# Kernel tuning notes

Measured on AMD Instinct MI355X. Metric: run time of the kernel, lower is better.

The kernel has to match this reference:

```python
import jax, jax.numpy as jnp
import numpy as np
from jax import lax

B, IMG, P, D, DEPTH = 32, 512, 16, 256, 8
G = IMG // P            # 32 grid side
N = G * G               # 1024 tokens
DQ = D // 8             # 32 (CCNet-style reduced q/k dim)
DF = 4 * D

# fixed Laplacian kernel for EdgeTokenExtractor (depthwise, HWIO with I=1)
_LAP = np.array([[0., -1., 0.], [-1., 4., -1.], [0., -1., 0.]], np.float32)


def setup_inputs() -> dict:
    key = jax.random.key(0)
    ks = jax.random.split(key, 16)
    s = 0.02
    return {
        'x': jax.random.normal(ks[0], (B, 1, IMG, IMG), jnp.float32),
        'w_patch': jax.random.normal(ks[1], (D, 1, P, P), jnp.float32) * s,
        'b_patch': jnp.zeros((D,), jnp.float32),
        'pos': jax.random.normal(ks[2], (1, N, D), jnp.float32) * s,
        'w_edge': jax.random.normal(ks[3], (D, D), jnp.float32) * s,
        'b_edge': jnp.zeros((D,), jnp.float32),
        'ln_g': jnp.ones((DEPTH, D), jnp.float32),
        'ln_b': jnp.zeros((DEPTH, D), jnp.float32),
        'wq': jax.random.normal(ks[4], (DEPTH, D, DQ), jnp.float32) * s,
        'bq': jnp.zeros((DEPTH, DQ), jnp.float32),
        'wk': jax.random.normal(ks[5], (DEPTH, D, DQ), jnp.float32) * s,
        'bk': jnp.zeros((DEPTH, DQ), jnp.float32),
        'wv': jax.random.normal(ks[6], (DEPTH, D, D), jnp.float32) * s,
        'bv': jnp.zeros((DEPTH, D), jnp.float32),
        'gamma': jnp.full((DEPTH,), 0.1, jnp.float32),
        'w1': jax.random.normal(ks[7], (DEPTH, D, DF), jnp.float32) * s,
        'b1': jnp.zeros((DEPTH, DF), jnp.float32),
        'w2': jax.random.normal(ks[8], (DEPTH, DF, D), jnp.float32) * s,
        'b2': jnp.zeros((DEPTH, D), jnp.float32),
        'w_head': jax.random.normal(ks[9], (D, 1), jnp.float32) * s,
        'b_head': jnp.zeros((1,), jnp.float32),
    }


def _ln(x, g, b):
    m = x.mean(-1, keepdims=True)
    v = ((x - m) ** 2).mean(-1, keepdims=True)
    return (x - m) * lax.rsqrt(v + 1e-5) * g + b


def _criss_cross(xn, wq, bq, wk, bk, wv, bv, gamma):
    # xn: [B,N,D] -> grid [B,G,G,D]; each token attends to its row + column.
    b_ = xn.shape[0]
    grid = xn.reshape(b_, G, G, D)
    q = grid @ wq + bq            # [B,G,G,DQ]
    k = grid @ wk + bk
    v = grid @ wv + bv            # [B,G,G,D]
    scale = 1.0 / np.sqrt(DQ).astype(np.float32)
    row = jnp.einsum('bhwc,bhvc->bhwv', q, k) * scale   # attend along width
    col = jnp.einsum('bhwc,buwc->bhwu', q, k) * scale   # attend along height
    # mask the duplicated self position in the column branch (CCNet trick)
    col = col - 1e9 * jnp.eye(G, dtype=col.dtype)[:, None, :]
    a = jax.nn.softmax(jnp.concatenate([row, col], axis=-1), axis=-1)  # [B,G,G,2G]
    out = (jnp.einsum('bhwv,bhvc->bhwc', a[..., :G], v)
           + jnp.einsum('bhwu,buwc->bhwc', a[..., G:], v))
    return (gamma * out + grid).reshape(b_, N, D)


def _edge_tokens(t, w_edge, b_edge):
    # depthwise Laplacian over the token grid, then linear + tanh
    b_ = t.shape[0]
    grid = t.reshape(b_, G, G, D)
    kern = jnp.tile(jnp.asarray(_LAP).reshape(3, 3, 1, 1), (1, 1, 1, D))  # [3,3,1,D]
    e = lax.conv_general_dilated(grid, kern, (1, 1), 'SAME',
                                 dimension_numbers=('NHWC', 'HWIO', 'NHWC'),
                                 feature_group_count=D)
    return jnp.tanh(e.reshape(b_, N, D) @ w_edge + b_edge)


def reference(x, w_patch, b_patch, pos, w_edge, b_edge, ln_g, ln_b,
              wq, bq, wk, bk, wv, bv, gamma, w1, b1, w2, b2, w_head, b_head):
    b_ = x.shape[0]
    # patch embed: conv stride=patch -> [B,D,G,G] -> [B,N,D]
    t = lax.conv_general_dilated(x, w_patch, (P, P), 'VALID',
                                 dimension_numbers=('NCHW', 'OIHW', 'NCHW'))
    t = t + b_patch[None, :, None, None]
    t = t.reshape(b_, D, N).transpose(0, 2, 1)
    t = t + pos
    t = t + _edge_tokens(t, w_edge, b_edge)

    def block(h, p):
        lg, lb, wq_, bq_, wk_, bk_, wv_, bv_, gm, w1_, b1_, w2_, b2_ = p
        # NOTE: original block reuses the SAME LayerNorm params for both sublayers
        h = h + _criss_cross(_ln(h, lg, lb), wq_, bq_, wk_, bk_, wv_, bv_, gm)
        hn = _ln(h, lg, lb)
        h = h + jax.nn.gelu(hn @ w1_ + b1_, approximate=False) @ w2_ + b2_
        return h, None

    t, _ = lax.scan(block, t, (ln_g, ln_b, wq, bq, wk, bk, wv, bv, gamma, w1, b1, w2, b2))
    out = t @ w_head + b_head                      # [B,N,1]
    return out.transpose(0, 2, 1).reshape(b_, 1, G, G)
```

## Files before the change

### kernel.cpp

```cpp
#include <hip/hip_runtime.h>
#include <hip/hip_bf16.h>

#define BB   32
#define IMG  512
#define PP   16
#define DD   256
#define GG   32
#define NN   1024
#define DQ_  32
#define DF_  1024
#define DEPTH_ 8

using short8  = __attribute__((ext_vector_type(8))) short;
using floatx4 = __attribute__((ext_vector_type(4))) float;

__device__ __forceinline__ float bu2f(unsigned short u) {
    return __uint_as_float(((unsigned int)u) << 16);
}
__device__ __forceinline__ unsigned short f2b(float f) {
    unsigned int u = __float_as_uint(f);
    u += 0x7fffu + ((u >> 16) & 1u);
    return (unsigned short)(u >> 16);
}
__device__ __forceinline__ float gelu_exact(float x) {
    return 0.5f * x * (1.0f + erff(x * 0.70710678118654752440f));
}
__device__ __forceinline__ float lo16(unsigned int u) {
    return __uint_as_float(u << 16);
}
__device__ __forceinline__ float hi16(unsigned int u) {
    return __uint_as_float(u & 0xffff0000u);
}
__device__ __forceinline__ float dot8(uint4 a, uint4 b) {
    const unsigned int* pa = (const unsigned int*)&a;
    const unsigned int* pb = (const unsigned int*)&b;
    float s = 0.f;
    #pragma unroll
    for (int i = 0; i < 4; ++i)
        s += lo16(pa[i]) * lo16(pb[i]) + hi16(pa[i]) * hi16(pb[i]);
    return s;
}

__global__ __launch_bounds__(256) void k_wtrans(const float* __restrict__ in,
                                                unsigned short* __restrict__ out,
                                                int R, int C) {
    __shared__ float tile[32][33];
    const int l = blockIdx.z;
    const int r0 = blockIdx.x * 32, c0 = blockIdx.y * 32;
    const int tx = threadIdx.x & 31, ty = threadIdx.x >> 5;
    const float* src = in + (size_t)l * R * C;
    unsigned short* dst = out + (size_t)l * R * C;
    #pragma unroll
    for (int i = 0; i < 4; ++i)
        tile[ty + i * 8][tx] = src[(size_t)(r0 + ty + i * 8) * C + c0 + tx];
    __syncthreads();
    #pragma unroll
    for (int i = 0; i < 4; ++i)
        dst[(size_t)(c0 + ty + i * 8) * R + r0 + tx] = f2b(tile[tx][ty + i * 8]);
}

__global__ __launch_bounds__(256) void k_qktrans(const float* __restrict__ wq,
                                                 const float* __restrict__ wk,
                                                 unsigned short* __restrict__ o) {
    const int l = blockIdx.z, j = blockIdx.x, k = threadIdx.x;
    float v = (j < 32) ? wq[(size_t)l * 8192 + k * 32 + j]
                       : wk[(size_t)l * 8192 + k * 32 + (j - 32)];
    o[((size_t)l * 64 + j) * 256 + k] = f2b(v);
}

__global__ void k_bqk(const float* __restrict__ bq, const float* __restrict__ bk,
                      float* __restrict__ o) {
    const int l = blockIdx.x, j = threadIdx.x;
    o[l * 64 + j] = (j < 32) ? bq[l * 32 + j] : bk[l * 32 + (j - 32)];
}

__global__ __launch_bounds__(256) void k_cvt(const float* __restrict__ in,
                                             unsigned short* __restrict__ out) {
    int i = blockIdx.x * 256 + threadIdx.x;
    out[i] = f2b(in[i]);
}

__global__ __launch_bounds__(256) void k_im2col(const float* __restrict__ x,
                                                unsigned short* __restrict__ xp) {
    const int tok = blockIdx.x;
    const int b  = tok >> 10;
    const int n  = tok & (NN - 1);
    const int gi = n >> 5, gj = n & 31;
    const int pi = threadIdx.x >> 4, pj = threadIdx.x & 15;
    xp[(size_t)tok * 256 + threadIdx.x] =
        f2b(x[(size_t)(b * IMG + gi * PP + pi) * IMG + gj * PP + pj]);
}

template <int K, int N, int MODE>
__global__ __launch_bounds__(256) void k_gemm(
    const unsigned short* __restrict__ A, const unsigned short* __restrict__ Bt,
    const float* __restrict__ bias, unsigned short* __restrict__ Cb,
    float* __restrict__ Cf, const float* __restrict__ pos) {
    __shared__ alignas(16) unsigned short As[64 * 32];
    __shared__ alignas(16) unsigned short Bs[64 * 32];
    const int t  = threadIdx.x;
    const int m0 = blockIdx.x * 64, n0 = blockIdx.y * 64;
    const int row = t >> 2, ch = t & 3;
    const unsigned short* ga = A  + (size_t)(m0 + row) * K + ch * 8;
    const unsigned short* gb = Bt + (size_t)(n0 + row) * K + ch * 8;

    const int lane = t & 63, wid = t >> 6;
    const int quad = lane >> 4, r = lane & 15;
    const int wm = (wid >> 1) * 32, wn = (wid & 1) * 32;

    floatx4 acc00 = {0.f, 0.f, 0.f, 0.f}, acc01 = {0.f, 0.f, 0.f, 0.f};
    floatx4 acc10 = {0.f, 0.f, 0.f, 0.f}, acc11 = {0.f, 0.f, 0.f, 0.f};

    uint4 ra = *(const uint4*)ga;
    uint4 rb = *(const uint4*)gb;
    const int KS = K / 32;
    for (int ks = 0; ks < KS; ++ks) {
        __syncthreads();
        *(uint4*)&As[t * 8] = ra;
        *(uint4*)&Bs[t * 8] = rb;
        __syncthreads();
        if (ks + 1 < KS) {
            ra = *(const uint4*)(ga + (ks + 1) * 32);
            rb = *(const uint4*)(gb + (ks + 1) * 32);
        }
        short8 a0 = *(const short8*)&As[(wm + r) * 32 + quad * 8];
        short8 a1 = *(const short8*)&As[(wm + 16 + r) * 32 + quad * 8];
        short8 b0 = *(const short8*)&Bs[(wn + r) * 32 + quad * 8];
        short8 b1 = *(const short8*)&Bs[(wn + 16 + r) * 32 + quad * 8];
        acc00 = __builtin_amdgcn_mfma_f32_16x16x32_bf16(a0, b0, acc00, 0, 0, 0);
        acc01 = __builtin_amdgcn_mfma_f32_16x16x32_bf16(a0, b1, acc01, 0, 0, 0);
        acc10 = __builtin_amdgcn_mfma_f32_16x16x32_bf16(a1, b0, acc10, 0, 0, 0);
        acc11 = __builtin_amdgcn_mfma_f32_16x16x32_bf16(a1, b1, acc11, 0, 0, 0);
    }
    const int nA = n0 + wn + r;
    const int nB = nA + 16;
    const float bias0 = bias[nA], bias1 = bias[nB];
    #pragma unroll
    for (int i = 0; i < 2; ++i) {
        floatx4 aj0 = i ? acc10 : acc00;
        floatx4 aj1 = i ? acc11 : acc01;
        const int mb = m0 + wm + i * 16 + quad * 4;
        #pragma unroll
        for (int g = 0; g < 4; ++g) {
            const int m = mb + g;
            float v0 = aj0[g] + bias0, v1 = aj1[g] + bias1;
            if (MODE == 0) {
                Cb[(size_t)m * N + nA] = f2b(gelu_exact(v0));
                Cb[(size_t)m * N + nB] = f2b(gelu_exact(v1));
            } else if (MODE == 1) {
                Cf[(size_t)m * N + nA] += v0;
                Cf[(size_t)m * N + nB] += v1;
            } else if (MODE == 2) {
                Cb[(size_t)m * N + nA] = f2b(v0);
                Cb[(size_t)m * N + nB] = f2b(v1);
            } else if (MODE == 3) {
                Cf[(size_t)m * N + nA] += tanhf(v0);
                Cf[(size_t)m * N + nB] += tanhf(v1);
            } else {
                Cf[(size_t)m * N + nA] = v0 + pos[(size_t)(m & (NN - 1)) * N + nA];
                Cf[(size_t)m * N + nB] = v1 + pos[(size_t)(m & (NN - 1)) * N + nB];
            }
        }
    }
}

__global__ __launch_bounds__(256) void k_lap(const float* __restrict__ h,
                                             unsigned short* __restrict__ e) {
    int idx = blockIdx.x * 256 + threadIdx.x;
    int n  = (idx >> 8) & (NN - 1);
    int gi = n >> 5, gj = n & 31;
    float c  = h[idx];
    float up = (gi > 0)  ? h[idx - GG * DD] : 0.f;
    float dn = (gi < 31) ? h[idx + GG * DD] : 0.f;
    float lf = (gj > 0)  ? h[idx - DD] : 0.f;
    float rt = (gj < 31) ? h[idx + DD] : 0.f;
    e[idx] = f2b(4.f * c - up - dn - lf - rt);
}

__global__ __launch_bounds__(256) void k_ln(
    const float* __restrict__ h, const float* __restrict__ g,
    const float* __restrict__ b, unsigned short* __restrict__ xnb, int layer) {
    const int wid = threadIdx.x >> 6, lane = threadIdx.x & 63;
    const int row = blockIdx.x * 4 + wid;
    const float4 xv = *(const float4*)(h + (size_t)row * DD + lane * 4);
    float s = xv.x + xv.y + xv.z + xv.w;
    #pragma unroll
    for (int o = 32; o; o >>= 1) s += __shfl_xor(s, o, 64);
    const float m = s * (1.f / 256.f);
    float t0 = xv.x - m, t1 = xv.y - m, t2 = xv.z - m, t3 = xv.w - m;
    float s2 = t0 * t0 + t1 * t1 + t2 * t2 + t3 * t3;
    #pragma unroll
    for (int o = 32; o; o >>= 1) s2 += __shfl_xor(s2, o, 64);
    const float r = rsqrtf(s2 * (1.f / 256.f) + 1e-5f);
    const int d0 = lane * 4;
    const float4 gv = *(const float4*)(g + layer * DD + d0);
    const float4 bv = *(const float4*)(b + layer * DD + d0);
    unsigned short* o = xnb + (size_t)row * DD + d0;
    o[0] = f2b(t0 * r * gv.x + bv.x);
    o[1] = f2b(t1 * r * gv.y + bv.y);
    o[2] = f2b(t2 * r * gv.z + bv.z);
    o[3] = f2b(t3 * r * gv.w + bv.w);
}

__global__ __launch_bounds__(256) void k_score(
    const unsigned short* __restrict__ qkb, unsigned short* __restrict__ P) {
    const int wid = threadIdx.x >> 6, lane = threadIdx.x & 63;
    const int tok = blockIdx.x * 4 + wid;
    const int b = tok >> 10, n = tok & (NN - 1);
    const int gi = n >> 5, gj = n & 31;
    const uint4* qp = (const uint4*)(qkb + (size_t)tok * 64);
    uint4 q0 = qp[0], q1 = qp[1], q2 = qp[2], q3 = qp[3];
    const int key = (lane < 32) ? (b * NN + gi * 32 + lane)
                                : (b * NN + (lane - 32) * 32 + gj);
    const uint4* kp = (const uint4*)(qkb + (size_t)key * 64 + 32);
    uint4 k0 = kp[0], k1 = kp[1], k2 = kp[2], k3 = kp[3];
    float s = dot8(q0, k0) + dot8(q1, k1) + dot8(q2, k2) + dot8(q3, k3);
    s *= 0.17677669529663687f;
    if (lane >= 32 && (lane - 32) == gi) s -= 1e9f;
    float m = s;
    #pragma unroll
    for (int o = 32; o; o >>= 1) m = fmaxf(m, __shfl_xor(m, o, 64));
    float e = expf(s - m);
    float sum = e;
    #pragma unroll
    for (int o = 32; o; o >>= 1) sum += __shfl_xor(sum, o, 64);
    P[(size_t)tok * 64 + lane] = f2b(e / sum);
}

__global__ __launch_bounds__(256) void k_avrow(
    const unsigned short* __restrict__ P, const unsigned short* __restrict__ v,
    const unsigned short* __restrict__ xnb, float* __restrict__ h,
    const float* __restrict__ gamma, int layer) {
    const int bgi = blockIdx.x;
    const int wid = threadIdx.x >> 6, lane = threadIdx.x & 63;
    const int d0 = lane * 4;
    uint2 vr[32];
    const unsigned short* vbase = v + ((size_t)bgi * 32) * 256 + d0;
    #pragma unroll
    for (int w = 0; w < 32; ++w) vr[w] = *(const uint2*)(vbase + (size_t)w * 256);
    const float g = gamma[layer];
    for (int j = 0; j < 8; ++j) {
        const int tok = bgi * 32 + wid * 8 + j;
        const uint4* pp = (const uint4*)(P + (size_t)tok * 64);
        unsigned int pa[16];
        *(uint4*)(pa)      = pp[0];
        *(uint4*)(pa + 4)  = pp[1];
        *(uint4*)(pa + 8)  = pp[2];
        *(uint4*)(pa + 12) = pp[3];
        float o0 = 0.f, o1 = 0.f, o2 = 0.f, o3 = 0.f;
        #pragma unroll
        for (int w = 0; w < 32; ++w) {
            float p = (w & 1) ? hi16(pa[w >> 1]) : lo16(pa[w >> 1]);
            o0 += p * lo16(vr[w].x); o1 += p * hi16(vr[w].x);
            o2 += p * lo16(vr[w].y); o3 += p * hi16(vr[w].y);
        }
        size_t idx = (size_t)tok * 256 + d0;
        uint2 xu = *(const uint2*)(xnb + idx);
        float4 hv = *(float4*)(h + idx);
        hv.x += lo16(xu.x) + g * o0; hv.y += hi16(xu.x) + g * o1;
        hv.z += lo16(xu.y) + g * o2; hv.w += hi16(xu.y) + g * o3;
        *(float4*)(h + idx) = hv;
    }
}

__global__ __launch_bounds__(256) void k_avcol(
    const unsigned short* __restrict__ P, const unsigned short* __restrict__ v,
    float* __restrict__ h, const float* __restrict__ gamma, int layer) {
    const int bgj = blockIdx.x;
    const int b = bgj >> 5, gj = bgj & 31;
    const int wid = threadIdx.x >> 6, lane = threadIdx.x & 63;
    const int d0 = lane * 4;
    uint2 vr[32];
    const unsigned short* vbase = v + ((size_t)b * NN + gj) * 256 + d0;
    #pragma unroll
    for (int u = 0; u < 32; ++u)
        vr[u] = *(const uint2*)(vbase + (size_t)u * 32 * 256);
    const float g = gamma[layer];
    for (int j = 0; j < 8; ++j) {
        const int gi = wid * 8 + j;
        const int tok = (b * 32 + gi) * 32 + gj;
        const uint4* pp = (const uint4*)(P + (size_t)tok * 64 + 32);
        unsigned int pa[16];
        *(uint4*)(pa)      = pp[0];
        *(uint4*)(pa + 4)  = pp[1];
        *(uint4*)(pa + 8)  = pp[2];
        *(uint4*)(pa + 12) = pp[3];
        float o0 = 0.f, o1 = 0.f, o2 = 0.f, o3 = 0.f;
        #pragma unroll
        for (int u = 0; u < 32; ++u) {
            float p = (u & 1) ? hi16(pa[u >> 1]) : lo16(pa[u >> 1]);
            o0 += p * lo16(vr[u].x); o1 += p * hi16(vr[u].x);
            o2 += p * lo16(vr[u].y); o3 += p * hi16(vr[u].y);
        }
        size_t idx = (size_t)tok * 256 + d0;
        float4 hv = *(float4*)(h + idx);
        hv.x += g * o0; hv.y += g * o1; hv.z += g * o2; hv.w += g * o3;
        *(float4*)(h + idx) = hv;
    }
}

__global__ __launch_bounds__(256) void k_head(
    const float* __restrict__ h, const float* __restrict__ wh,
    const float* __restrict__ bh, float* __restrict__ out) {
    const int tok  = blockIdx.x * 4 + (threadIdx.x >> 6);
    const int lane = threadIdx.x & 63;
    float acc = 0.f;
    #pragma unroll
    for (int i = 0; i < 4; ++i)
        acc += h[(size_t)tok * DD + lane + 64 * i] * wh[lane + 64 * i];
    #pragma unroll
    for (int o = 32; o; o >>= 1) acc += __shfl_down(acc, o, 64);
    if (lane == 0) out[tok] = acc + bh[0];
}

extern "C" void kernel_launch(void* const* d_in, const int* in_sizes, int n_in,
                              void* d_out, int out_size, void* d_ws, size_t ws_size,
                              hipStream_t stream) {
    const float* fx   = (const float*)d_in[0];
    const float* fwp  = (const float*)d_in[1];
    const float* fbp  = (const float*)d_in[2];
    const float* fpos = (const float*)d_in[3];
    const float* fwe  = (const float*)d_in[4];
    const float* fbe  = (const float*)d_in[5];
    const float* flg  = (const float*)d_in[6];
    const float* flb  = (const float*)d_in[7];
    const float* fwq  = (const float*)d_in[8];
    const float* fbq  = (const float*)d_in[9];
    const float* fwk  = (const float*)d_in[10];
    const float* fbk  = (const float*)d_in[11];
    const float* fwv  = (const float*)d_in[12];
    const float* fbv  = (const float*)d_in[13];
    const float* fgam = (const float*)d_in[14];
    const float* fw1  = (const float*)d_in[15];
    const float* fb1  = (const float*)d_in[16];
    const float* fw2  = (const float*)d_in[17];
    const float* fb2  = (const float*)d_in[18];
    const float* fwh  = (const float*)d_in[19];
    const float* fbh  = (const float*)d_in[20];
    float* out = (float*)d_out;

    float* ws = (float*)d_ws;
    float*          h    = ws;
    unsigned short* xnb  = (unsigned short*)(ws + 8388608);
    unsigned short* w1t  = (unsigned short*)(ws + 12582912);
    unsigned short* w2t  = (unsigned short*)(ws + 13631488);
    unsigned short* wvT  = (unsigned short*)(ws + 14680064);
    unsigned short* wqkT = (unsigned short*)(ws + 14942208);
    unsigned short* wpb  = (unsigned short*)(ws + 15007744);
    unsigned short* weT  = (unsigned short*)(ws + 15040512);
    float*          bqk  = ws + 15073280;
    float* S = ws + 15073792;
    unsigned short* qkb  = (unsigned short*)S;
    unsigned short* v    = (unsigned short*)(S + 1048576);
    unsigned short* P    = (unsigned short*)(S + 5242880);
    unsigned short* xp   = (unsigned short*)S;
    unsigned short* e    = (unsigned short*)S;
    unsigned short* Hc   = (unsigned short*)S;

    const int TOK = BB * NN;

    k_wtrans<<<dim3(8, 32, 8), 256, 0, stream>>>(fw1, w1t, 256, 1024);
    k_wtrans<<<dim3(32, 8, 8), 256, 0, stream>>>(fw2, w2t, 1024, 256);
    k_wtrans<<<dim3(8, 8, 8),  256, 0, stream>>>(fwv, wvT, 256, 256);
    k_wtrans<<<dim3(8, 8, 1),  256, 0, stream>>>(fwe, weT, 256, 256);
    k_qktrans<<<dim3(64, 1, 8), 256, 0, stream>>>(fwq, fwk, wqkT);
    k_bqk<<<8, 64, 0, stream>>>(fbq, fbk, bqk);
    k_cvt<<<256, 256, 0, stream>>>(fwp, wpb);

    k_im2col<<<TOK, 256, 0, stream>>>(fx, xp);
    k_gemm<256, 256, 4><<<dim3(512, 4), 256, 0, stream>>>(
        xp, wpb, fbp, nullptr, h, fpos);
    k_lap<<<TOK, 256, 0, stream>>>(h, e);
    k_gemm<256, 256, 3><<<dim3(512, 4), 256, 0, stream>>>(
        e, weT, fbe, nullptr, h, nullptr);

    for (int l = 0; l < DEPTH_; ++l) {
        k_ln<<<TOK / 4, 256, 0, stream>>>(h, flg, flb, xnb, l);
        k_gemm<256, 64, 2><<<dim3(512, 1), 256, 0, stream>>>(
            xnb, wqkT + (size_t)l * 16384, bqk + l * 64, qkb, nullptr, nullptr);
        k_gemm<256, 256, 2><<<dim3(512, 4), 256, 0, stream>>>(
            xnb, wvT + (size_t)l * 65536, fbv + l * 256, v, nullptr, nullptr);
        k_score<<<TOK / 4, 256, 0, stream>>>(qkb, P);
        k_avcol<<<BB * GG, 256, 0, stream>>>(P, v, h, fgam, l);
        k_avrow<<<BB * GG, 256, 0, stream>>>(P, v, xnb, h, fgam, l);
        k_ln<<<TOK / 4, 256, 0, stream>>>(h, flg, flb, xnb, l);
        for (int c = 0; c < 2; ++c) {
            k_gemm<256, 1024, 0><<<dim3(256, 16), 256, 0, stream>>>(
                xnb + (size_t)c * 16384 * 256, w1t + (size_t)l * 262144,
                fb1 + (size_t)l * 1024, Hc, nullptr, nullptr);
            k_gemm<1024, 256, 1><<<dim3(256, 4), 256, 0, stream>>>(
                Hc, w2t + (size_t)l * 262144,
                fb2 + (size_t)l * 256, nullptr, h + (size_t)c * 16384 * 256, nullptr);
        }
    }

    k_head<<<TOK / 4, 256, 0, stream>>>(h, fwh, fbh, out);
}
```

Measured before the change: 1.854 ms.

## Add 128x128 LDS-direct GEMM, fuse row attention with LayerNorm, split AV blocks

Adds a 128x128-tile GEMM kernel that loads tiles straight into LDS with global_load_lds and keeps a 4x4 MFMA accumulator grid per wave. All large GEMMs (patch embed, edge, V projection, both MLP GEMMs) now use it, which cuts global re-reads per FLOP. The row-attention accumulation is fused with the second LayerNorm so one pass over h disappears, the AV kernels are split into four times more blocks for occupancy, and LN stores are packed. The cost is higher register pressure from 64 accumulator floats and the 32-entry V register arrays, plus no software prefetch in the new GEMM loop.

```diff
diff --git a/kernel.cpp b/kernel.cpp
--- a/kernel.cpp
+++ b/kernel.cpp
@@ -22,6 +22,9 @@
     u += 0x7fffu + ((u >> 16) & 1u);
     return (unsigned short)(u >> 16);
 }
+__device__ __forceinline__ unsigned int pack2(float a, float b) {
+    return (unsigned int)f2b(a) | ((unsigned int)f2b(b) << 16);
+}
 __device__ __forceinline__ float gelu_exact(float x) {
     return 0.5f * x * (1.0f + erff(x * 0.70710678118654752440f));
 }
@@ -39,6 +42,11 @@
     for (int i = 0; i < 4; ++i)
         s += lo16(pa[i]) * lo16(pb[i]) + hi16(pa[i]) * hi16(pb[i]);
     return s;
+}
+__device__ __forceinline__ void gld16(unsigned short* lds, const unsigned short* g) {
+    __builtin_amdgcn_global_load_lds(
+        (const __attribute__((address_space(1))) void*)g,
+        (__attribute__((address_space(3))) void*)lds, 16, 0, 0);
 }
 
 __global__ __launch_bounds__(256) void k_wtrans(const float* __restrict__ in,
@@ -103,14 +111,10 @@
     const int row = t >> 2, ch = t & 3;
     const unsigned short* ga = A  + (size_t)(m0 + row) * K + ch * 8;
     const unsigned short* gb = Bt + (size_t)(n0 + row) * K + ch * 8;
-
     const int lane = t & 63, wid = t >> 6;
     const int quad = lane >> 4, r = lane & 15;
     const int wm = (wid >> 1) * 32, wn = (wid & 1) * 32;
-
-    floatx4 acc00 = {0.f, 0.f, 0.f, 0.f}, acc01 = {0.f, 0.f, 0.f, 0.f};
-    floatx4 acc10 = {0.f, 0.f, 0.f, 0.f}, acc11 = {0.f, 0.f, 0.f, 0.f};
-
+    floatx4 acc00 = {0,0,0,0}, acc01 = {0,0,0,0}, acc10 = {0,0,0,0}, acc11 = {0,0,0,0};
     uint4 ra = *(const uint4*)ga;
     uint4 rb = *(const uint4*)gb;
     const int KS = K / 32;
@@ -144,21 +148,78 @@
         for (int g = 0; g < 4; ++g) {
             const int m = mb + g;
             float v0 = aj0[g] + bias0, v1 = aj1[g] + bias1;
-            if (MODE == 0) {
-                Cb[(size_t)m * N + nA] = f2b(gelu_exact(v0));
-                Cb[(size_t)m * N + nB] = f2b(gelu_exact(v1));
-            } else if (MODE == 1) {
-                Cf[(size_t)m * N + nA] += v0;
-                Cf[(size_t)m * N + nB] += v1;
-            } else if (MODE == 2) {
+            if (MODE == 2) {
                 Cb[(size_t)m * N + nA] = f2b(v0);
                 Cb[(size_t)m * N + nB] = f2b(v1);
-            } else if (MODE == 3) {
-                Cf[(size_t)m * N + nA] += tanhf(v0);
-                Cf[(size_t)m * N + nB] += tanhf(v1);
-            } else {
-                Cf[(size_t)m * N + nA] = v0 + pos[(size_t)(m & (NN - 1)) * N + nA];
-                Cf[(size_t)m * N + nB] = v1 + pos[(size_t)(m & (NN - 1)) * N + nB];
+            }
+        }
+    }
+}
+
+template <int K, int N, int MODE>
+__global__ __launch_bounds__(256) void k_gemm128(
+    const unsigned short* __restrict__ A, const unsigned short* __restrict__ Bt,
+    const float* __restrict__ bias, unsigned short* __restrict__ Cb,
+    float* __restrict__ Cf, const float* __restrict__ pos) {
+    __shared__ alignas(16) unsigned short As[128 * 32];
+    __shared__ alignas(16) unsigned short Bs[128 * 32];
+    const int t  = threadIdx.x;
+    const int m0 = blockIdx.x * 128, n0 = blockIdx.y * 128;
+    const int row = t >> 2, ch = t & 3;
+    const unsigned short* gA0 = A  + (size_t)(m0 + row) * K + ch * 8;
+    const unsigned short* gA1 = A  + (size_t)(m0 + 64 + row) * K + ch * 8;
+    const unsigned short* gB0 = Bt + (size_t)(n0 + row) * K + ch * 8;
+    const unsigned short* gB1 = Bt + (size_t)(n0 + 64 + row) * K + ch * 8;
+
+    const int lane = t & 63, wid = t >> 6;
+    const int quad = lane >> 4, r = lane & 15;
+    const int wm = (wid >> 1) * 64, wn = (wid & 1) * 64;
+
+    floatx4 acc[4][4];
+    #pragma unroll
+    for (int i = 0; i < 4; ++i)
+        #pragma unroll
+        for (int n = 0; n < 4; ++n) acc[i][n] = floatx4{0.f, 0.f, 0.f, 0.f};
+
+    const int KS = K / 32;
+    for (int ks = 0; ks < KS; ++ks) {
+        __syncthreads();
+        gld16(&As[t * 8],        gA0 + ks * 32);
+        gld16(&As[2048 + t * 8], gA1 + ks * 32);
+        gld16(&Bs[t * 8],        gB0 + ks * 32);
+        gld16(&Bs[2048 + t * 8], gB1 + ks * 32);
+        __syncthreads();
+        short8 a[4], b[4];
+        #pragma unroll
+        for (int i = 0; i < 4; ++i)
+            a[i] = *(const short8*)&As[(wm + i * 16 + r) * 32 + quad * 8];
+        #pragma unroll
+        for (int n = 0; n < 4; ++n)
+            b[n] = *(const short8*)&Bs[(wn + n * 16 + r) * 32 + quad * 8];
+        #pragma unroll
+        for (int i = 0; i < 4; ++i)
+            #pragma unroll
+            for (int n = 0; n < 4; ++n)
+                acc[i][n] = __builtin_amdgcn_mfma_f32_16x16x32_bf16(
+                    a[i], b[n], acc[i][n], 0, 0, 0);
+    }
+    #pragma unroll
+    for (int n = 0; n < 4; ++n) {
+        const int col = n0 + wn + n * 16 + r;
+        const float bs = bias[col];
+        #pragma unroll
+        for (int i = 0; i < 4; ++i) {
+            const int mb = m0 + wm + i * 16 + quad * 4;
+            #pragma unroll
+            for (int g = 0; g < 4; ++g) {
+                const int m = mb + g;
+                float v0 = acc[i][n][g] + bs;
+                if (MODE == 0)      Cb[(size_t)m * N + col] = f2b(gelu_exact(v0));
+                else if (MODE == 1) Cf[(size_t)m * N + col] += v0;
+                else if (MODE == 2) Cb[(size_t)m * N + col] = f2b(v0);
+                else if (MODE == 3) Cf[(size_t)m * N + col] += tanhf(v0);
+                else Cf[(size_t)m * N + col] =
+                         v0 + pos[(size_t)(m & (NN - 1)) * N + col];
             }
         }
     }
@@ -195,11 +256,10 @@
     const int d0 = lane * 4;
     const float4 gv = *(const float4*)(g + layer * DD + d0);
     const float4 bv = *(const float4*)(b + layer * DD + d0);
-    unsigned short* o = xnb + (size_t)row * DD + d0;
-    o[0] = f2b(t0 * r * gv.x + bv.x);
-    o[1] = f2b(t1 * r * gv.y + bv.y);
-    o[2] = f2b(t2 * r * gv.z + bv.z);
-    o[3] = f2b(t3 * r * gv.w + bv.w);
+    uint2 outp;
+    outp.x = pack2(t0 * r * gv.x + bv.x, t1 * r * gv.y + bv.y);
+    outp.y = pack2(t2 * r * gv.z + bv.z, t3 * r * gv.w + bv.w);
+    *(uint2*)(xnb + (size_t)row * DD + d0) = outp;
 }
 
 __global__ __launch_bounds__(256) void k_score(
@@ -227,75 +287,111 @@
     P[(size_t)tok * 64 + lane] = f2b(e / sum);
 }
 
-__global__ __launch_bounds__(256) void k_avrow(
+__global__ __launch_bounds__(256) void k_avcol(
     const unsigned short* __restrict__ P, const unsigned short* __restrict__ v,
-    const unsigned short* __restrict__ xnb, float* __restrict__ h,
-    const float* __restrict__ gamma, int layer) {
-    const int bgi = blockIdx.x;
+    float* __restrict__ h, const float* __restrict__ gamma, int layer) {
+    const int idx = blockIdx.x;
+    const int b = idx >> 7, gj = (idx >> 2) & 31, oct = idx & 3;
     const int wid = threadIdx.x >> 6, lane = threadIdx.x & 63;
     const int d0 = lane * 4;
     uint2 vr[32];
-    const unsigned short* vbase = v + ((size_t)bgi * 32) * 256 + d0;
-    #pragma unroll
-    for (int w = 0; w < 32; ++w) vr[w] = *(const uint2*)(vbase + (size_t)w * 256);
+    const unsigned short* vbase = v + ((size_t)(b * NN + gj)) * 256 + d0;
+    #pragma unroll
+    for (int u = 0; u < 32; ++u)
+        vr[u] = *(const uint2*)(vbase + (size_t)u * 32 * 256);
     const float g = gamma[layer];
-    for (int j = 0; j < 8; ++j) {
-        const int tok = bgi * 32 + wid * 8 + j;
-        const uint4* pp = (const uint4*)(P + (size_t)tok * 64);
-        unsigned int pa[16];
-        *(uint4*)(pa)      = pp[0];
-        *(uint4*)(pa + 4)  = pp[1];
-        *(uint4*)(pa + 8)  = pp[2];
-        *(uint4*)(pa + 12) = pp[3];
+    size_t hidx[2];
+    float4 hv[2];
+    unsigned int pa[2][16];
+    #pragma unroll
+    for (int jj = 0; jj < 2; ++jj) {
+        const int gi = oct * 8 + wid * 2 + jj;
+        const int tok = b * NN + gi * 32 + gj;
+        hidx[jj] = (size_t)tok * 256 + d0;
+        const uint4* pp = (const uint4*)(P + (size_t)tok * 64 + 32);
+        *(uint4*)(pa[jj])      = pp[0];
+        *(uint4*)(pa[jj] + 4)  = pp[1];
+        *(uint4*)(pa[jj] + 8)  = pp[2];
+        *(uint4*)(pa[jj] + 12) = pp[3];
+        hv[jj] = *(const float4*)(h + hidx[jj]);
+    }
+    #pragma unroll
+    for (int jj = 0; jj < 2; ++jj) {
         float o0 = 0.f, o1 = 0.f, o2 = 0.f, o3 = 0.f;
         #pragma unroll
-        for (int w = 0; w < 32; ++w) {
-            float p = (w & 1) ? hi16(pa[w >> 1]) : lo16(pa[w >> 1]);
-            o0 += p * lo16(vr[w].x); o1 += p * hi16(vr[w].x);
-            o2 += p * lo16(vr[w].y); o3 += p * hi16(vr[w].y);
-        }
-        size_t idx = (size_t)tok * 256 + d0;
-        uint2 xu = *(const uint2*)(xnb + idx);
-        float4 hv = *(float4*)(h + idx);
-        hv.x += lo16(xu.x) + g * o0; hv.y += hi16(xu.x) + g * o1;
-        hv.z += lo16(xu.y) + g * o2; hv.w += hi16(xu.y) + g * o3;
-        *(float4*)(h + idx) = hv;
-    }
-}
-
-__global__ __launch_bounds__(256) void k_avcol(
+        for (int u = 0; u < 32; ++u) {
+            float p = (u & 1) ? hi16(pa[jj][u >> 1]) : lo16(pa[jj][u >> 1]);
+            o0 += p * lo16(vr[u].x); o1 += p * hi16(vr[u].x);
+            o2 += p * lo16(vr[u].y); o3 += p * hi16(vr[u].y);
+        }
+        float4 r = hv[jj];
+        r.x += g * o0; r.y += g * o1; r.z += g * o2; r.w += g * o3;
+        *(float4*)(h + hidx[jj]) = r;
+    }
+}
+
+__global__ __launch_bounds__(256) void k_avrow_ln(
     const unsigned short* __restrict__ P, const unsigned short* __restrict__ v,
-    float* __restrict__ h, const float* __restrict__ gamma, int layer) {
-    const int bgj = blockIdx.x;
-    const int b = bgj >> 5, gj = bgj & 31;
+    float* __restrict__ h, unsigned short* __restrict__ xnb,
+    const float* __restrict__ gamma, const float* __restrict__ lg,
+    const float* __restrict__ lb, int layer) {
+    const int idx = blockIdx.x;
+    const int b = idx >> 7, gi = (idx >> 2) & 31, oct = idx & 3;
     const int wid = threadIdx.x >> 6, lane = threadIdx.x & 63;
     const int d0 = lane * 4;
     uint2 vr[32];
-    const unsigned short* vbase = v + ((size_t)b * NN + gj) * 256 + d0;
-    #pragma unroll
-    for (int u = 0; u < 32; ++u)
-        vr[u] = *(const uint2*)(vbase + (size_t)u * 32 * 256);
+    const unsigned short* vbase = v + ((size_t)(b * NN + gi * 32)) * 256 + d0;
+    #pragma unroll
+    for (int w = 0; w < 32; ++w)
+        vr[w] = *(const uint2*)(vbase + (size_t)w * 256);
     const float g = gamma[layer];
-    for (int j = 0; j < 8; ++j) {
-        const int gi = wid * 8 + j;
-        const int tok = (b * 32 + gi) * 32 + gj;
-        const uint4* pp = (const uint4*)(P + (size_t)tok * 64 + 32);
-        unsigned int pa[16];
-        *(uint4*)(pa)      = pp[0];
-        *(uint4*)(pa + 4)  = pp[1];
-        *(uint4*)(pa + 8)  = pp[2];
-        *(uint4*)(pa + 12) = pp[3];
+    const float4 gv = *(const float4*)(lg + layer * DD + d0);
+    const float4 bv = *(const float4*)(lb + layer * DD + d0);
+    size_t hidx[2];
+    float4 hv[2];
+    uint2 xu[2];
+    unsigned int pa[2][16];
+    #pragma unroll
+    for (int jj = 0; jj < 2; ++jj) {
+        const int gj = oct * 8 + wid * 2 + jj;
+        const int tok = b * NN + gi * 32 + gj;
+        hidx[jj] = (size_t)tok * 256 + d0;
+        const uint4* pp = (const uint4*)(P + (size_t)tok * 64);
+        *(uint4*)(pa[jj])      = pp[0];
+        *(uint4*)(pa[jj] + 4)  = pp[1];
+        *(uint4*)(pa[jj] + 8)  = pp[2];
+        *(uint4*)(pa[jj] + 12) = pp[3];
+        hv[jj] = *(const float4*)(h + hidx[jj]);
+        xu[jj] = *(const uint2*)(xnb + hidx[jj]);
+    }
+    #pragma unroll
+    for (int jj = 0; jj < 2; ++jj) {
         float o0 = 0.f, o1 = 0.f, o2 = 0.f, o3 = 0.f;
         #pragma unroll
-        for (int u = 0; u < 32; ++u) {
-            float p = (u & 1) ? hi16(pa[u >> 1]) : lo16(pa[u >> 1]);
-            o0 += p * lo16(vr[u].x); o1 += p * hi16(vr[u].x);
-            o2 += p * lo16(vr[u].y); o3 += p * hi16(vr[u].y);
-        }
-        size_t idx = (size_t)tok * 256 + d0;
-        float4 hv = *(float4*)(h + idx);
-        hv.x += g * o0; hv.y += g * o1; hv.z += g * o2; hv.w += g * o3;
-        *(float4*)(h + idx) = hv;
+        for (int w = 0; w < 32; ++w) {
+            float p = (w & 1) ? hi16(pa[jj][w >> 1]) : lo16(pa[jj][w >> 1]);
+            o0 += p * lo16(vr[w].x); o1 += p * hi16(vr[w].x);
+            o2 += p * lo16(vr[w].y); o3 += p * hi16(vr[w].y);
+        }
+        float f0 = hv[jj].x + lo16(xu[jj].x) + g * o0;
+        float f1 = hv[jj].y + hi16(xu[jj].x) + g * o1;
+        float f2 = hv[jj].z + lo16(xu[jj].y) + g * o2;
+        float f3 = hv[jj].w + hi16(xu[jj].y) + g * o3;
+        float s = f0 + f1 + f2 + f3;
+        #pragma unroll
+        for (int o = 32; o; o >>= 1) s += __shfl_xor(s, o, 64);
+        const float m = s * (1.f / 256.f);
+        float t0 = f0 - m, t1 = f1 - m, t2 = f2 - m, t3 = f3 - m;
+        float s2 = t0 * t0 + t1 * t1 + t2 * t2 + t3 * t3;
+        #pragma unroll
+        for (int o = 32; o; o >>= 1) s2 += __shfl_xor(s2, o, 64);
+        const float r = rsqrtf(s2 * (1.f / 256.f) + 1e-5f);
+        float4 hvout = {f0, f1, f2, f3};
+        *(float4*)(h + hidx[jj]) = hvout;
+        uint2 outp;
+        outp.x = pack2(t0 * r * gv.x + bv.x, t1 * r * gv.y + bv.y);
+        outp.y = pack2(t2 * r * gv.z + bv.z, t3 * r * gv.w + bv.w);
+        *(uint2*)(xnb + hidx[jj]) = outp;
     }
 }
 
@@ -368,27 +464,26 @@
     k_cvt<<<256, 256, 0, stream>>>(fwp, wpb);
 
     k_im2col<<<TOK, 256, 0, stream>>>(fx, xp);
-    k_gemm<256, 256, 4><<<dim3(512, 4), 256, 0, stream>>>(
+    k_gemm128<256, 256, 4><<<dim3(256, 2), 256, 0, stream>>>(
         xp, wpb, fbp, nullptr, h, fpos);
     k_lap<<<TOK, 256, 0, stream>>>(h, e);
-    k_gemm<256, 256, 3><<<dim3(512, 4), 256, 0, stream>>>(
+    k_gemm128<256, 256, 3><<<dim3(256, 2), 256, 0, stream>>>(
         e, weT, fbe, nullptr, h, nullptr);
 
     for (int l = 0; l < DEPTH_; ++l) {
         k_ln<<<TOK / 4, 256, 0, stream>>>(h, flg, flb, xnb, l);
         k_gemm<256, 64, 2><<<dim3(512, 1), 256, 0, stream>>>(
             xnb, wqkT + (size_t)l * 16384, bqk + l * 64, qkb, nullptr, nullptr);
-        k_gemm<256, 256, 2><<<dim3(512, 4), 256, 0, stream>>>(
+        k_gemm128<256, 256, 2><<<dim3(256, 2), 256, 0, stream>>>(
             xnb, wvT + (size_t)l * 65536, fbv + l * 256, v, nullptr, nullptr);
         k_score<<<TOK / 4, 256, 0, stream>>>(qkb, P);
-        k_avcol<<<BB * GG, 256, 0, stream>>>(P, v, h, fgam, l);
-        k_avrow<<<BB * GG, 256, 0, stream>>>(P, v, xnb, h, fgam, l);
-        k_ln<<<TOK / 4, 256, 0, stream>>>(h, flg, flb, xnb, l);
+        k_avcol<<<4096, 256, 0, stream>>>(P, v, h, fgam, l);
+        k_avrow_ln<<<4096, 256, 0, stream>>>(P, v, h, xnb, fgam, flg, flb, l);
         for (int c = 0; c < 2; ++c) {
-            k_gemm<256, 1024, 0><<<dim3(256, 16), 256, 0, stream>>>(
+            k_gemm128<256, 1024, 0><<<dim3(128, 8), 256, 0, stream>>>(
                 xnb + (size_t)c * 16384 * 256, w1t + (size_t)l * 262144,
                 fb1 + (size_t)l * 1024, Hc, nullptr, nullptr);
-            k_gemm<1024, 256, 1><<<dim3(256, 4), 256, 0, stream>>>(
+            k_gemm128<1024, 256, 1><<<dim3(128, 2), 256, 0, stream>>>(
                 Hc, w2t + (size_t)l * 262144,
                 fb2 + (size_t)l * 256, nullptr, h + (size_t)c * 16384 * 256, nullptr);
         }
```

After: 1.961 ms. +5.8%, slower.
